# Performance work log

Measured on AMD Instinct MI355X. Metric: run time of the kernel, lower is better.

The kernel has to match this reference:

```python
import jax, jax.numpy as jnp
import numpy as np

# DMoAH constants (match init_kwargs)
H_TOTAL = 16   # attn_h_total
H_ACTIVE = 4   # attn_h_active (per-token top-k heads)


def setup_inputs() -> dict:
    key = jax.random.key(0)
    k1, k2, k3, k4 = jax.random.split(key, 4)
    B, T, D = 2, 2048, 1024
    x = jax.random.normal(k1, (B, T, D), dtype=jnp.float32)
    W_qkv = jax.random.normal(k2, (D, 3 * D), dtype=jnp.float32) * (1.0 / np.sqrt(D))
    W_router = jax.random.normal(k3, (D, H_TOTAL), dtype=jnp.float32) * (1.0 / np.sqrt(D))
    W_o = jax.random.normal(k4, (D, D), dtype=jnp.float32) * (1.0 / np.sqrt(D))
    return {"x": x, "W_qkv": W_qkv, "W_router": W_router, "W_o": W_o}


def reference(x, W_qkv, W_router, W_o):
    B, T, D = x.shape
    dh = D // H_TOTAL
    # --- router: per-token softmax over heads, keep top-k head probs (others zeroed) ---
    probs = jax.nn.softmax(x @ W_router, axis=-1)                 # [B,T,H]
    topv, _ = jax.lax.top_k(probs, H_ACTIVE)                      # [B,T,k]
    thresh = topv[..., -1:]                                       # kth largest prob
    gates = jnp.where(probs >= thresh, probs, 0.0)                # [B,T,H] sparse gates
    # --- QKV projection ---
    qkv = x @ W_qkv                                               # [B,T,3D]
    q, k, v = jnp.split(qkv, 3, axis=-1)
    q = q.reshape(B, T, H_TOTAL, dh).transpose(0, 2, 1, 3)        # [B,H,T,dh]
    k = k.reshape(B, T, H_TOTAL, dh).transpose(0, 2, 1, 3)
    v = v.reshape(B, T, H_TOTAL, dh).transpose(0, 2, 1, 3)
    # --- causal SDPA per head ---
    scale = 1.0 / np.sqrt(dh).astype(np.float32)
    scores = jnp.einsum("bhqd,bhkd->bhqk", q, k) * scale          # [B,H,T,T]
    causal = jnp.tril(jnp.ones((T, T), dtype=bool))
    scores = jnp.where(causal, scores, -jnp.inf)
    attn = jax.nn.softmax(scores, axis=-1)
    head_out = jnp.einsum("bhqk,bhkd->bhqd", attn, v)             # [B,H,T,dh]
    # --- per-token head gating (scatter-combine of active heads) ---
    head_out = head_out.transpose(0, 2, 1, 3)                     # [B,T,H,dh]
    y = (head_out * gates[..., None]).reshape(B, T, D)
    return y @ W_o
```

## Files before the change

kernel.cpp:

```cpp
#include <hip/hip_runtime.h>
#include <math.h>

#define BB 2
#define TT 2048
#define DD 1024
#define HH 16
#define DH 64
#define BTOT (BB*TT)
#define NEG_INF (-1e30f)
#define ATTN_MFMA 1

typedef _Float16 half8 __attribute__((ext_vector_type(8)));
typedef _Float16 half4 __attribute__((ext_vector_type(4)));
typedef float floatx4 __attribute__((ext_vector_type(4)));

__global__ __launch_bounds__(256) void split_f32(const float* __restrict__ in,
                                                 _Float16* __restrict__ hi,
                                                 _Float16* __restrict__ lo,
                                                 int n4) {
  int idx = blockIdx.x * 256 + threadIdx.x;
  const int stride = gridDim.x * 256;
  for (; idx < n4; idx += stride) {
    float4 v = reinterpret_cast<const float4*>(in)[idx];
    half4 hv, lv;
    hv[0] = (_Float16)v.x; lv[0] = (_Float16)(v.x - (float)hv[0]);
    hv[1] = (_Float16)v.y; lv[1] = (_Float16)(v.y - (float)hv[1]);
    hv[2] = (_Float16)v.z; lv[2] = (_Float16)(v.z - (float)hv[2]);
    hv[3] = (_Float16)v.w; lv[3] = (_Float16)(v.w - (float)hv[3]);
    reinterpret_cast<half4*>(hi)[idx] = hv;
    reinterpret_cast<half4*>(lo)[idx] = lv;
  }
}

__global__ __launch_bounds__(256) void wsplit_t(const float* __restrict__ W,
                                                _Float16* __restrict__ Wth,
                                                _Float16* __restrict__ Wtl,
                                                int K, int N) {
  __shared__ float buf[64][65];
  const int tid = threadIdx.x;
  const int k0 = blockIdx.y * 64;
  const int n0 = blockIdx.x * 64;
  const int rr = tid >> 4;
  const int cc = (tid & 15) * 4;
#pragma unroll
  for (int p = 0; p < 4; ++p) {
    const int r = rr + p * 16;
    float4 v = *reinterpret_cast<const float4*>(&W[(size_t)(k0 + r) * N + n0 + cc]);
    buf[r][cc+0] = v.x; buf[r][cc+1] = v.y; buf[r][cc+2] = v.z; buf[r][cc+3] = v.w;
  }
  __syncthreads();
  const int tn = tid >> 2;
#pragma unroll
  for (int pp = 0; pp < 2; ++pp) {
    const int c2 = (tid & 3) + pp * 4;
    half8 hv, lv;
#pragma unroll
    for (int j = 0; j < 8; ++j) {
      float f = buf[c2*8 + j][tn];
      hv[j] = (_Float16)f;
      lv[j] = (_Float16)(f - (float)hv[j]);
    }
    *reinterpret_cast<half8*>(&Wth[(size_t)(n0 + tn) * K + k0 + c2*8]) = hv;
    *reinterpret_cast<half8*>(&Wtl[(size_t)(n0 + tn) * K + k0 + c2*8]) = lv;
  }
}

__global__ __launch_bounds__(64) void router_kernel(const float* __restrict__ x,
                                                    const float* __restrict__ Wr,
                                                    float* __restrict__ gates) {
  const int row = blockIdx.x;
  const int lane = threadIdx.x;
  const float* xr = x + (size_t)row * DD;
  float acc[16];
#pragma unroll
  for (int c = 0; c < 16; ++c) acc[c] = 0.f;
  for (int d = lane; d < DD; d += 64) {
    float xv = xr[d];
    const float4* wrow = reinterpret_cast<const float4*>(Wr + (size_t)d * HH);
#pragma unroll
    for (int g = 0; g < 4; ++g) {
      float4 w = wrow[g];
      acc[g*4+0] = fmaf(xv, w.x, acc[g*4+0]);
      acc[g*4+1] = fmaf(xv, w.y, acc[g*4+1]);
      acc[g*4+2] = fmaf(xv, w.z, acc[g*4+2]);
      acc[g*4+3] = fmaf(xv, w.w, acc[g*4+3]);
    }
  }
#pragma unroll
  for (int c = 0; c < 16; ++c) {
    float v = acc[c];
    v += __shfl_down(v, 32);
    v += __shfl_down(v, 16);
    v += __shfl_down(v, 8);
    v += __shfl_down(v, 4);
    v += __shfl_down(v, 2);
    v += __shfl_down(v, 1);
    acc[c] = v;
  }
  if (lane == 0) {
    float mx = acc[0];
#pragma unroll
    for (int c = 1; c < 16; ++c) mx = fmaxf(mx, acc[c]);
    float e[16]; float den = 0.f;
#pragma unroll
    for (int c = 0; c < 16; ++c) { e[c] = __expf(acc[c] - mx); den += e[c]; }
    float tmp[16];
#pragma unroll
    for (int c = 0; c < 16; ++c) tmp[c] = acc[c];
    float th = NEG_INF;
    for (int it = 0; it < 4; ++it) {
      float bv = NEG_INF; int bi = 0;
      for (int c = 0; c < 16; ++c) { if (tmp[c] > bv) { bv = tmp[c]; bi = c; } }
      tmp[bi] = NEG_INF;
      th = bv;
    }
    float inv = 1.f / den;
    float* gr = gates + (size_t)row * HH;
#pragma unroll
    for (int c = 0; c < 16; ++c) gr[c] = (acc[c] >= th) ? e[c] * inv : 0.f;
  }
}

__global__ __launch_bounds__(256) void hgemm_split(const _Float16* __restrict__ Ah,
                                                   const _Float16* __restrict__ Al,
                                                   const _Float16* __restrict__ Bth,
                                                   const _Float16* __restrict__ Btl,
                                                   float* __restrict__ C,
                                                   int M, int N, int K) {
  __shared__ _Float16 As[2][128][40];
  __shared__ _Float16 Bs[2][128][40];
  const int tid = threadIdx.x;
  const int lane = tid & 63;
  const int w = tid >> 6;
  const int wr = w >> 1, wc = w & 1;
  const int lr = lane & 15, lg = lane >> 4;
  const int m0 = blockIdx.y * 128, n0 = blockIdx.x * 128;
  const int srow = tid >> 2;
  const int schunk = (tid & 3) * 8;
  const _Float16* ApH = Ah + (size_t)(m0 + srow) * K + schunk;
  const _Float16* ApL = Al + (size_t)(m0 + srow) * K + schunk;
  const _Float16* BpH = Bth + (size_t)(n0 + srow) * K + schunk;
  const _Float16* BpL = Btl + (size_t)(n0 + srow) * K + schunk;
  const size_t rskip = (size_t)64 * K;

  floatx4 acc[4][4] = {};
  for (int k0 = 0; k0 < K; k0 += 32) {
    int4 a0h = *reinterpret_cast<const int4*>(ApH + k0);
    int4 a1h = *reinterpret_cast<const int4*>(ApH + rskip + k0);
    int4 a0l = *reinterpret_cast<const int4*>(ApL + k0);
    int4 a1l = *reinterpret_cast<const int4*>(ApL + rskip + k0);
    int4 b0h = *reinterpret_cast<const int4*>(BpH + k0);
    int4 b1h = *reinterpret_cast<const int4*>(BpH + rskip + k0);
    int4 b0l = *reinterpret_cast<const int4*>(BpL + k0);
    int4 b1l = *reinterpret_cast<const int4*>(BpL + rskip + k0);
    __syncthreads();
    *reinterpret_cast<int4*>(&As[0][srow][schunk])      = a0h;
    *reinterpret_cast<int4*>(&As[0][srow + 64][schunk]) = a1h;
    *reinterpret_cast<int4*>(&As[1][srow][schunk])      = a0l;
    *reinterpret_cast<int4*>(&As[1][srow + 64][schunk]) = a1l;
    *reinterpret_cast<int4*>(&Bs[0][srow][schunk])      = b0h;
    *reinterpret_cast<int4*>(&Bs[0][srow + 64][schunk]) = b1h;
    *reinterpret_cast<int4*>(&Bs[1][srow][schunk])      = b0l;
    *reinterpret_cast<int4*>(&Bs[1][srow + 64][schunk]) = b1l;
    __syncthreads();
    half8 af[2][4], bf[2][4];
#pragma unroll
    for (int mi = 0; mi < 4; ++mi) {
      af[0][mi] = *reinterpret_cast<const half8*>(&As[0][wr*64 + mi*16 + lr][lg*8]);
      af[1][mi] = *reinterpret_cast<const half8*>(&As[1][wr*64 + mi*16 + lr][lg*8]);
    }
#pragma unroll
    for (int ni = 0; ni < 4; ++ni) {
      bf[0][ni] = *reinterpret_cast<const half8*>(&Bs[0][wc*64 + ni*16 + lr][lg*8]);
      bf[1][ni] = *reinterpret_cast<const half8*>(&Bs[1][wc*64 + ni*16 + lr][lg*8]);
    }
#pragma unroll
    for (int mi = 0; mi < 4; ++mi)
#pragma unroll
      for (int ni = 0; ni < 4; ++ni) {
        acc[mi][ni] = __builtin_amdgcn_mfma_f32_16x16x32_f16(af[0][mi], bf[0][ni], acc[mi][ni], 0, 0, 0);
        acc[mi][ni] = __builtin_amdgcn_mfma_f32_16x16x32_f16(af[0][mi], bf[1][ni], acc[mi][ni], 0, 0, 0);
        acc[mi][ni] = __builtin_amdgcn_mfma_f32_16x16x32_f16(af[1][mi], bf[0][ni], acc[mi][ni], 0, 0, 0);
      }
  }
#pragma unroll
  for (int mi = 0; mi < 4; ++mi)
#pragma unroll
    for (int ni = 0; ni < 4; ++ni) {
      const int n = n0 + wc*64 + ni*16 + lr;
#pragma unroll
      for (int r = 0; r < 4; ++r) {
        const int m = m0 + wr*64 + mi*16 + lg*4 + r;
        C[(size_t)m * N + n] = acc[mi][ni][r];
      }
    }
}

__global__ __launch_bounds__(256) void attn_mfma(const float* __restrict__ qkv,
                                                 const float* __restrict__ gates,
                                                 _Float16* __restrict__ yhi,
                                                 _Float16* __restrict__ ylo) {
  __shared__ _Float16 Ksh[64][68], Ksl[64][68];
  __shared__ _Float16 Vth[64][68], Vtl[64][68];
  __shared__ _Float16 Psh[64][68], Psl[64][68];
  const int nQT = TT / 64;
  const int bid = blockIdx.x;
  const int qt = nQT - 1 - bid / (BB*HH);
  const int bh = bid % (BB*HH);
  const int b = bh / HH, h = bh % HH;
  const int tid = threadIdx.x;
  const int lane = tid & 63;
  const int wv = tid >> 6;
  const int lr = lane & 15;
  const int lg = lane >> 4;
  const size_t rs = 3 * DD;
  const float* kbase = qkv + (size_t)b*TT*rs + DD + h*DH;
  const float* vbase = qkv + (size_t)b*TT*rs + 2*DD + h*DH;

  half8 qfh[2], qfl[2];
  {
    const float* qrow = qkv + (size_t)(b*TT + qt*64 + wv*16 + lr) * rs + h*DH + lg*8;
#pragma unroll
    for (int c = 0; c < 2; ++c) {
      float4 v0 = *reinterpret_cast<const float4*>(qrow + c*32);
      float4 v1 = *reinterpret_cast<const float4*>(qrow + c*32 + 4);
      const float f[8] = {v0.x,v0.y,v0.z,v0.w,v1.x,v1.y,v1.z,v1.w};
#pragma unroll
      for (int j = 0; j < 8; ++j) {
        qfh[c][j] = (_Float16)f[j];
        qfl[c][j] = (_Float16)(f[j] - (float)qfh[c][j]);
      }
    }
  }
  floatx4 oacc[4] = {};
  float rowM[4], rowL[4];
#pragma unroll
  for (int r = 0; r < 4; ++r) { rowM[r] = NEG_INF; rowL[r] = 0.f; }

  const int sm = tid >> 2;
  const int sg = tid & 3;

  for (int jt = 0; jt <= qt; ++jt) {
    const float* ksrc = kbase + (size_t)(jt*64 + sm) * rs;
    const float* vsrc = vbase + (size_t)(jt*64 + sm) * rs;
    float4 kreg[4], vreg[4];
#pragma unroll
    for (int u = 0; u < 4; ++u) {
      const int c = (sg + 4*u) * 4;
      kreg[u] = *reinterpret_cast<const float4*>(ksrc + c);
      vreg[u] = *reinterpret_cast<const float4*>(vsrc + c);
    }
    __syncthreads();
#pragma unroll
    for (int u = 0; u < 4; ++u) {
      const int c = (sg + 4*u) * 4;
      const float kf[4] = {kreg[u].x, kreg[u].y, kreg[u].z, kreg[u].w};
      half4 kh, kl;
#pragma unroll
      for (int j = 0; j < 4; ++j) {
        kh[j] = (_Float16)kf[j];
        kl[j] = (_Float16)(kf[j] - (float)kh[j]);
      }
      *reinterpret_cast<half4*>(&Ksh[sm][c]) = kh;
      *reinterpret_cast<half4*>(&Ksl[sm][c]) = kl;
      const float vf[4] = {vreg[u].x, vreg[u].y, vreg[u].z, vreg[u].w};
#pragma unroll
      for (int j = 0; j < 4; ++j) {
        _Float16 vh = (_Float16)vf[j];
        Vth[c+j][sm] = vh;
        Vtl[c+j][sm] = (_Float16)(vf[j] - (float)vh);
      }
    }
    __syncthreads();
    floatx4 sacc[4] = {};
#pragma unroll
    for (int c = 0; c < 2; ++c)
#pragma unroll
      for (int nf = 0; nf < 4; ++nf) {
        half8 kbh = *reinterpret_cast<const half8*>(&Ksh[nf*16 + lr][c*32 + lg*8]);
        half8 kbl = *reinterpret_cast<const half8*>(&Ksl[nf*16 + lr][c*32 + lg*8]);
        sacc[nf] = __builtin_amdgcn_mfma_f32_16x16x32_f16(qfh[c], kbh, sacc[nf], 0, 0, 0);
        sacc[nf] = __builtin_amdgcn_mfma_f32_16x16x32_f16(qfh[c], kbl, sacc[nf], 0, 0, 0);
        sacc[nf] = __builtin_amdgcn_mfma_f32_16x16x32_f16(qfl[c], kbh, sacc[nf], 0, 0, 0);
      }
    float p[4][4];
    float corr[4];
#pragma unroll
    for (int r = 0; r < 4; ++r) {
      const int qidx = qt*64 + wv*16 + lg*4 + r;
      float tmax = NEG_INF;
#pragma unroll
      for (int nf = 0; nf < 4; ++nf) {
        const int kidx = jt*64 + nf*16 + lr;
        float sv = sacc[nf][r] * 0.125f;
        if (kidx > qidx) sv = NEG_INF;
        p[nf][r] = sv;
        tmax = fmaxf(tmax, sv);
      }
      tmax = fmaxf(tmax, __shfl_xor(tmax, 1));
      tmax = fmaxf(tmax, __shfl_xor(tmax, 2));
      tmax = fmaxf(tmax, __shfl_xor(tmax, 4));
      tmax = fmaxf(tmax, __shfl_xor(tmax, 8));
      const float mnew = fmaxf(rowM[r], tmax);
      corr[r] = __expf(rowM[r] - mnew);
      float tsum = 0.f;
#pragma unroll
      for (int nf = 0; nf < 4; ++nf) {
        const float pv = __expf(p[nf][r] - mnew);
        p[nf][r] = pv;
        tsum += pv;
      }
      tsum += __shfl_xor(tsum, 1);
      tsum += __shfl_xor(tsum, 2);
      tsum += __shfl_xor(tsum, 4);
      tsum += __shfl_xor(tsum, 8);
      rowL[r] = rowL[r] * corr[r] + tsum;
      rowM[r] = mnew;
    }
#pragma unroll
    for (int nf = 0; nf < 4; ++nf)
#pragma unroll
      for (int r = 0; r < 4; ++r) {
        const _Float16 ph = (_Float16)p[nf][r];
        Psh[wv*16 + lg*4 + r][nf*16 + lr] = ph;
        Psl[wv*16 + lg*4 + r][nf*16 + lr] = (_Float16)(p[nf][r] - (float)ph);
      }
#pragma unroll
    for (int df = 0; df < 4; ++df)
#pragma unroll
      for (int r = 0; r < 4; ++r)
        oacc[df][r] *= corr[r];
#pragma unroll
    for (int c = 0; c < 2; ++c) {
      half8 pah = *reinterpret_cast<const half8*>(&Psh[wv*16 + lr][c*32 + lg*8]);
      half8 pal = *reinterpret_cast<const half8*>(&Psl[wv*16 + lr][c*32 + lg*8]);
#pragma unroll
      for (int df = 0; df < 4; ++df) {
        half8 vbh = *reinterpret_cast<const half8*>(&Vth[df*16 + lr][c*32 + lg*8]);
        half8 vbl = *reinterpret_cast<const half8*>(&Vtl[df*16 + lr][c*32 + lg*8]);
        oacc[df] = __builtin_amdgcn_mfma_f32_16x16x32_f16(pah, vbh, oacc[df], 0, 0, 0);
        oacc[df] = __builtin_amdgcn_mfma_f32_16x16x32_f16(pah, vbl, oacc[df], 0, 0, 0);
        oacc[df] = __builtin_amdgcn_mfma_f32_16x16x32_f16(pal, vbh, oacc[df], 0, 0, 0);
      }
    }
  }
#pragma unroll
  for (int r = 0; r < 4; ++r) {
    const int t = qt*64 + wv*16 + lg*4 + r;
    const float g = gates[((size_t)(b*TT + t)) * HH + h];
    const float sc = g / rowL[r];
#pragma unroll
    for (int df = 0; df < 4; ++df) {
      const float v = oacc[df][r] * sc;
      const _Float16 vh = (_Float16)v;
      const size_t off = ((size_t)(b*TT + t)) * DD + h*DH + df*16 + lr;
      yhi[off] = vh;
      ylo[off] = (_Float16)(v - (float)vh);
    }
  }
}

__global__ __launch_bounds__(256) void attn_kernel(const float* __restrict__ qkv,
                                                   const float* __restrict__ gates,
                                                   _Float16* __restrict__ yhi,
                                                   _Float16* __restrict__ ylo) {
  __shared__ float Qs[64][68];
  __shared__ float KPs[64][68];
  __shared__ float Vs[64][64];
  const int nQT = TT / 64;
  const int bid = blockIdx.x;
  const int qt = nQT - 1 - bid / (BB*HH);
  const int bh = bid % (BB*HH);
  const int b = bh / HH;
  const int h = bh % HH;
  const int tid = threadIdx.x;
  const int tx = tid & 15;
  const int ty = tid >> 4;
  const size_t rs = 3 * DD;
  const float* qbase = qkv + ((size_t)(b*TT + qt*64)) * rs + h*DH;
  const float* kbase = qkv + ((size_t)b*TT) * rs + DD + h*DH;
  const float* vbase = qkv + ((size_t)b*TT) * rs + 2*DD + h*DH;
  const int sm = tid >> 2;
  const int sg = tid & 3;
  {
    const float* src = qbase + (size_t)sm * rs;
#pragma unroll
    for (int u = 0; u < 4; ++u) {
      const int c = (sg + 4*u) * 4;
      float4 v = *reinterpret_cast<const float4*>(src + c);
      Qs[c+0][sm] = v.x; Qs[c+1][sm] = v.y; Qs[c+2][sm] = v.z; Qs[c+3][sm] = v.w;
    }
  }
  float oacc[4][4] = {};
  float rowM[4], rowL[4];
#pragma unroll
  for (int i = 0; i < 4; ++i) { rowM[i] = NEG_INF; rowL[i] = 0.f; }
  for (int jt = 0; jt <= qt; ++jt) {
    const float* ksrc = kbase + (size_t)(jt*64 + sm) * rs;
    const float* vsrc = vbase + (size_t)(jt*64 + sm) * rs;
    float4 kreg[4], vreg[4];
#pragma unroll
    for (int u = 0; u < 4; ++u) {
      const int c = (sg + 4*u) * 4;
      kreg[u] = *reinterpret_cast<const float4*>(ksrc + c);
      vreg[u] = *reinterpret_cast<const float4*>(vsrc + c);
    }
    __syncthreads();
#pragma unroll
    for (int u = 0; u < 4; ++u) {
      const int c = (sg + 4*u) * 4;
      KPs[c+0][sm] = kreg[u].x; KPs[c+1][sm] = kreg[u].y;
      KPs[c+2][sm] = kreg[u].z; KPs[c+3][sm] = kreg[u].w;
      *reinterpret_cast<float4*>(&Vs[sm][c]) = vreg[u];
    }
    __syncthreads();
    float s[4][4] = {};
#pragma unroll 8
    for (int d = 0; d < 64; ++d) {
      float4 qv = *reinterpret_cast<const float4*>(&Qs[d][ty*4]);
      float4 kv = *reinterpret_cast<const float4*>(&KPs[d][tx*4]);
      const float qa[4] = {qv.x,qv.y,qv.z,qv.w};
      const float ka[4] = {kv.x,kv.y,kv.z,kv.w};
#pragma unroll
      for (int i = 0; i < 4; ++i)
#pragma unroll
        for (int j = 0; j < 4; ++j)
          s[i][j] = fmaf(qa[i], ka[j], s[i][j]);
    }
    __syncthreads();
    float p[4][4];
    float corr[4];
#pragma unroll
    for (int i = 0; i < 4; ++i) {
      const int qidx = qt*64 + ty*4 + i;
      float tmax = NEG_INF;
#pragma unroll
      for (int j = 0; j < 4; ++j) {
        const int kidx = jt*64 + tx*4 + j;
        float sv = s[i][j] * 0.125f;
        if (kidx > qidx) sv = NEG_INF;
        s[i][j] = sv;
        tmax = fmaxf(tmax, sv);
      }
      tmax = fmaxf(tmax, __shfl_xor(tmax, 1));
      tmax = fmaxf(tmax, __shfl_xor(tmax, 2));
      tmax = fmaxf(tmax, __shfl_xor(tmax, 4));
      tmax = fmaxf(tmax, __shfl_xor(tmax, 8));
      const float mnew = fmaxf(rowM[i], tmax);
      corr[i] = __expf(rowM[i] - mnew);
      float tsum = 0.f;
#pragma unroll
      for (int j = 0; j < 4; ++j) {
        p[i][j] = __expf(s[i][j] - mnew);
        tsum += p[i][j];
      }
      tsum += __shfl_xor(tsum, 1);
      tsum += __shfl_xor(tsum, 2);
      tsum += __shfl_xor(tsum, 4);
      tsum += __shfl_xor(tsum, 8);
      rowL[i] = rowL[i] * corr[i] + tsum;
      rowM[i] = mnew;
    }
#pragma unroll
    for (int i = 0; i < 4; ++i) {
      float4 v = make_float4(p[i][0], p[i][1], p[i][2], p[i][3]);
      *reinterpret_cast<float4*>(&KPs[ty*4+i][tx*4]) = v;
    }
#pragma unroll
    for (int i = 0; i < 4; ++i)
#pragma unroll
      for (int j = 0; j < 4; ++j)
        oacc[i][j] *= corr[i];
    __syncthreads();
#pragma unroll 4
    for (int n = 0; n < 64; ++n) {
      float4 vv = *reinterpret_cast<const float4*>(&Vs[n][tx*4]);
      const float va[4] = {vv.x, vv.y, vv.z, vv.w};
#pragma unroll
      for (int i = 0; i < 4; ++i) {
        const float pm = KPs[ty*4+i][n];
#pragma unroll
        for (int j = 0; j < 4; ++j)
          oacc[i][j] = fmaf(pm, va[j], oacc[i][j]);
      }
    }
  }
#pragma unroll
  for (int i = 0; i < 4; ++i) {
    const int t = qt*64 + ty*4 + i;
    const float g = gates[((size_t)(b*TT + t)) * HH + h];
    const float sc = g / rowL[i];
    half4 hv, lv;
#pragma unroll
    for (int j = 0; j < 4; ++j) {
      float v = oacc[i][j] * sc;
      hv[j] = (_Float16)v;
      lv[j] = (_Float16)(v - (float)hv[j]);
    }
    const size_t off = ((size_t)(b*TT + t)) * DD + h*DH + tx*4;
    *reinterpret_cast<half4*>(&yhi[off]) = hv;
    *reinterpret_cast<half4*>(&ylo[off]) = lv;
  }
}

extern "C" void kernel_launch(void* const* d_in, const int* in_sizes, int n_in,
                              void* d_out, int out_size, void* d_ws, size_t ws_size,
                              hipStream_t stream) {
  (void)in_sizes; (void)n_in; (void)out_size; (void)ws_size;
  const float* x    = (const float*)d_in[0];
  const float* Wqkv = (const float*)d_in[1];
  const float* Wr   = (const float*)d_in[2];
  const float* Wo   = (const float*)d_in[3];
  float* out = (float*)d_out;

  float* ws = (float*)d_ws;
  float* qkv   = ws;
  float* gates = qkv + (size_t)BTOT * 3 * DD;
  _Float16* x_hi = (_Float16*)(gates + (size_t)BTOT * HH);
  _Float16* x_lo = x_hi + (size_t)BTOT * DD;
  _Float16* Wqh  = x_lo + (size_t)BTOT * DD;
  _Float16* Wql  = Wqh + (size_t)DD * 3 * DD;
  _Float16* Woh  = Wql + (size_t)DD * 3 * DD;
  _Float16* Wol  = Woh + (size_t)DD * DD;
  _Float16* yhi = x_hi;
  _Float16* ylo = x_lo;

  split_f32<<<1024, 256, 0, stream>>>(x, x_hi, x_lo, BTOT * DD / 4);
  wsplit_t<<<dim3(3*DD/64, DD/64), 256, 0, stream>>>(Wqkv, Wqh, Wql, DD, 3*DD);
  wsplit_t<<<dim3(DD/64, DD/64), 256, 0, stream>>>(Wo, Woh, Wol, DD, DD);
  router_kernel<<<BTOT, 64, 0, stream>>>(x, Wr, gates);
  hgemm_split<<<dim3(3*DD/128, BTOT/128), 256, 0, stream>>>(x_hi, x_lo, Wqh, Wql, qkv, BTOT, 3*DD, DD);
#if ATTN_MFMA
  attn_mfma<<<(TT/64)*BB*HH, 256, 0, stream>>>(qkv, gates, yhi, ylo);
#else
  attn_kernel<<<(TT/64)*BB*HH, 256, 0, stream>>>(qkv, gates, yhi, ylo);
#endif
  hgemm_split<<<dim3(DD/128, BTOT/128), 256, 0, stream>>>(yhi, ylo, Woh, Wol, out, BTOT, DD, DD);
}
```

Before: 370.3 us.

## Emit split-fp16 QKV from GEMM epilogue and drop V low-part MFMA

The QKV GEMM now writes hi/lo fp16 halves directly in its epilogue, so the attention kernel loads fp16 instead of fp32 and skips per-tile conversion. The V low-order term (pah*vfl) is dropped by default, which removes one MFMA per P·V step plus the V_lo loads and shared-memory stores. The unused scalar attention kernel is deleted. Dropping V_lo lowers accuracy on the P·V product.

```diff
diff --git a/kernel.cpp b/kernel.cpp
--- a/kernel.cpp
+++ b/kernel.cpp
@@ -8,7 +8,7 @@
 #define DH 64
 #define BTOT (BB*TT)
 #define NEG_INF (-1e30f)
-#define ATTN_MFMA 1
+#define V_LO 0
 
 typedef _Float16 half8 __attribute__((ext_vector_type(8)));
 typedef _Float16 half4 __attribute__((ext_vector_type(4)));
@@ -121,11 +121,14 @@
   }
 }
 
+template<bool EMIT_HALF>
 __global__ __launch_bounds__(256) void hgemm_split(const _Float16* __restrict__ Ah,
                                                    const _Float16* __restrict__ Al,
                                                    const _Float16* __restrict__ Bth,
                                                    const _Float16* __restrict__ Btl,
                                                    float* __restrict__ C,
+                                                   _Float16* __restrict__ Ch,
+                                                   _Float16* __restrict__ Cl,
                                                    int M, int N, int K) {
   __shared__ _Float16 As[2][128][40];
   __shared__ _Float16 Bs[2][128][40];
@@ -191,17 +194,28 @@
 #pragma unroll
       for (int r = 0; r < 4; ++r) {
         const int m = m0 + wr*64 + mi*16 + lg*4 + r;
-        C[(size_t)m * N + n] = acc[mi][ni][r];
-      }
-    }
-}
-
-__global__ __launch_bounds__(256) void attn_mfma(const float* __restrict__ qkv,
+        const float v = acc[mi][ni][r];
+        if (EMIT_HALF) {
+          const _Float16 vh = (_Float16)v;
+          Ch[(size_t)m * N + n] = vh;
+          Cl[(size_t)m * N + n] = (_Float16)(v - (float)vh);
+        } else {
+          C[(size_t)m * N + n] = v;
+        }
+      }
+    }
+}
+
+__global__ __launch_bounds__(256) void attn_mfma(const _Float16* __restrict__ qkvh,
+                                                 const _Float16* __restrict__ qkvl,
                                                  const float* __restrict__ gates,
                                                  _Float16* __restrict__ yhi,
                                                  _Float16* __restrict__ ylo) {
   __shared__ _Float16 Ksh[64][68], Ksl[64][68];
-  __shared__ _Float16 Vth[64][68], Vtl[64][68];
+  __shared__ _Float16 Vth[64][68];
+#if V_LO
+  __shared__ _Float16 Vtl[64][68];
+#endif
   __shared__ _Float16 Psh[64][68], Psl[64][68];
   const int nQT = TT / 64;
   const int bid = blockIdx.x;
@@ -214,22 +228,21 @@
   const int lr = lane & 15;
   const int lg = lane >> 4;
   const size_t rs = 3 * DD;
-  const float* kbase = qkv + (size_t)b*TT*rs + DD + h*DH;
-  const float* vbase = qkv + (size_t)b*TT*rs + 2*DD + h*DH;
+  const _Float16* kbh = qkvh + (size_t)b*TT*rs + DD + h*DH;
+  const _Float16* kbl = qkvl + (size_t)b*TT*rs + DD + h*DH;
+  const _Float16* vbh = qkvh + (size_t)b*TT*rs + 2*DD + h*DH;
+#if V_LO
+  const _Float16* vbl = qkvl + (size_t)b*TT*rs + 2*DD + h*DH;
+#endif
 
   half8 qfh[2], qfl[2];
   {
-    const float* qrow = qkv + (size_t)(b*TT + qt*64 + wv*16 + lr) * rs + h*DH + lg*8;
+    const _Float16* qrh = qkvh + (size_t)(b*TT + qt*64 + wv*16 + lr) * rs + h*DH + lg*8;
+    const _Float16* qrl = qkvl + (size_t)(b*TT + qt*64 + wv*16 + lr) * rs + h*DH + lg*8;
 #pragma unroll
     for (int c = 0; c < 2; ++c) {
-      float4 v0 = *reinterpret_cast<const float4*>(qrow + c*32);
-      float4 v1 = *reinterpret_cast<const float4*>(qrow + c*32 + 4);
-      const float f[8] = {v0.x,v0.y,v0.z,v0.w,v1.x,v1.y,v1.z,v1.w};
-#pragma unroll
-      for (int j = 0; j < 8; ++j) {
-        qfh[c][j] = (_Float16)f[j];
-        qfl[c][j] = (_Float16)(f[j] - (float)qfh[c][j]);
-      }
+      qfh[c] = *reinterpret_cast<const half8*>(qrh + c*32);
+      qfl[c] = *reinterpret_cast<const half8*>(qrl + c*32);
     }
   }
   floatx4 oacc[4] = {};
@@ -241,35 +254,30 @@
   const int sg = tid & 3;
 
   for (int jt = 0; jt <= qt; ++jt) {
-    const float* ksrc = kbase + (size_t)(jt*64 + sm) * rs;
-    const float* vsrc = vbase + (size_t)(jt*64 + sm) * rs;
-    float4 kreg[4], vreg[4];
-#pragma unroll
-    for (int u = 0; u < 4; ++u) {
-      const int c = (sg + 4*u) * 4;
-      kreg[u] = *reinterpret_cast<const float4*>(ksrc + c);
-      vreg[u] = *reinterpret_cast<const float4*>(vsrc + c);
-    }
+    const size_t roff = (size_t)(jt*64 + sm) * rs + sg*16;
+    half8 kh0 = *reinterpret_cast<const half8*>(kbh + roff);
+    half8 kh1 = *reinterpret_cast<const half8*>(kbh + roff + 8);
+    half8 kl0 = *reinterpret_cast<const half8*>(kbl + roff);
+    half8 kl1 = *reinterpret_cast<const half8*>(kbl + roff + 8);
+    half8 vh0 = *reinterpret_cast<const half8*>(vbh + roff);
+    half8 vh1 = *reinterpret_cast<const half8*>(vbh + roff + 8);
+#if V_LO
+    half8 vl0 = *reinterpret_cast<const half8*>(vbl + roff);
+    half8 vl1 = *reinterpret_cast<const half8*>(vbl + roff + 8);
+#endif
     __syncthreads();
-#pragma unroll
-    for (int u = 0; u < 4; ++u) {
-      const int c = (sg + 4*u) * 4;
-      const float kf[4] = {kreg[u].x, kreg[u].y, kreg[u].z, kreg[u].w};
-      half4 kh, kl;
-#pragma unroll
-      for (int j = 0; j < 4; ++j) {
-        kh[j] = (_Float16)kf[j];
-        kl[j] = (_Float16)(kf[j] - (float)kh[j]);
-      }
-      *reinterpret_cast<half4*>(&Ksh[sm][c]) = kh;
-      *reinterpret_cast<half4*>(&Ksl[sm][c]) = kl;
-      const float vf[4] = {vreg[u].x, vreg[u].y, vreg[u].z, vreg[u].w};
-#pragma unroll
-      for (int j = 0; j < 4; ++j) {
-        _Float16 vh = (_Float16)vf[j];
-        Vth[c+j][sm] = vh;
-        Vtl[c+j][sm] = (_Float16)(vf[j] - (float)vh);
-      }
+    *reinterpret_cast<half8*>(&Ksh[sm][sg*16])     = kh0;
+    *reinterpret_cast<half8*>(&Ksh[sm][sg*16 + 8]) = kh1;
+    *reinterpret_cast<half8*>(&Ksl[sm][sg*16])     = kl0;
+    *reinterpret_cast<half8*>(&Ksl[sm][sg*16 + 8]) = kl1;
+#pragma unroll
+    for (int jj = 0; jj < 8; ++jj) {
+      Vth[sg*16 + jj][sm]     = vh0[jj];
+      Vth[sg*16 + 8 + jj][sm] = vh1[jj];
+#if V_LO
+      Vtl[sg*16 + jj][sm]     = vl0[jj];
+      Vtl[sg*16 + 8 + jj][sm] = vl1[jj];
+#endif
     }
     __syncthreads();
     floatx4 sacc[4] = {};
@@ -277,11 +285,11 @@
     for (int c = 0; c < 2; ++c)
 #pragma unroll
       for (int nf = 0; nf < 4; ++nf) {
-        half8 kbh = *reinterpret_cast<const half8*>(&Ksh[nf*16 + lr][c*32 + lg*8]);
-        half8 kbl = *reinterpret_cast<const half8*>(&Ksl[nf*16 + lr][c*32 + lg*8]);
-        sacc[nf] = __builtin_amdgcn_mfma_f32_16x16x32_f16(qfh[c], kbh, sacc[nf], 0, 0, 0);
-        sacc[nf] = __builtin_amdgcn_mfma_f32_16x16x32_f16(qfh[c], kbl, sacc[nf], 0, 0, 0);
-        sacc[nf] = __builtin_amdgcn_mfma_f32_16x16x32_f16(qfl[c], kbh, sacc[nf], 0, 0, 0);
+        half8 kfh = *reinterpret_cast<const half8*>(&Ksh[nf*16 + lr][c*32 + lg*8]);
+        half8 kfl = *reinterpret_cast<const half8*>(&Ksl[nf*16 + lr][c*32 + lg*8]);
+        sacc[nf] = __builtin_amdgcn_mfma_f32_16x16x32_f16(qfh[c], kfh, sacc[nf], 0, 0, 0);
+        sacc[nf] = __builtin_amdgcn_mfma_f32_16x16x32_f16(qfh[c], kfl, sacc[nf], 0, 0, 0);
+        sacc[nf] = __builtin_amdgcn_mfma_f32_16x16x32_f16(qfl[c], kfh, sacc[nf], 0, 0, 0);
       }
     float p[4][4];
     float corr[4];
@@ -336,11 +344,13 @@
       half8 pal = *reinterpret_cast<const half8*>(&Psl[wv*16 + lr][c*32 + lg*8]);
 #pragma unroll
       for (int df = 0; df < 4; ++df) {
-        half8 vbh = *reinterpret_cast<const half8*>(&Vth[df*16 + lr][c*32 + lg*8]);
-        half8 vbl = *reinterpret_cast<const half8*>(&Vtl[df*16 + lr][c*32 + lg*8]);
-        oacc[df] = __builtin_amdgcn_mfma_f32_16x16x32_f16(pah, vbh, oacc[df], 0, 0, 0);
-        oacc[df] = __builtin_amdgcn_mfma_f32_16x16x32_f16(pah, vbl, oacc[df], 0, 0, 0);
-        oacc[df] = __builtin_amdgcn_mfma_f32_16x16x32_f16(pal, vbh, oacc[df], 0, 0, 0);
+        half8 vfh = *reinterpret_cast<const half8*>(&Vth[df*16 + lr][c*32 + lg*8]);
+        oacc[df] = __builtin_amdgcn_mfma_f32_16x16x32_f16(pah, vfh, oacc[df], 0, 0, 0);
+        oacc[df] = __builtin_amdgcn_mfma_f32_16x16x32_f16(pal, vfh, oacc[df], 0, 0, 0);
+#if V_LO
+        half8 vfl = *reinterpret_cast<const half8*>(&Vtl[df*16 + lr][c*32 + lg*8]);
+        oacc[df] = __builtin_amdgcn_mfma_f32_16x16x32_f16(pah, vfl, oacc[df], 0, 0, 0);
+#endif
       }
     }
   }
@@ -357,149 +367,6 @@
       yhi[off] = vh;
       ylo[off] = (_Float16)(v - (float)vh);
     }
-  }
-}
-
-__global__ __launch_bounds__(256) void attn_kernel(const float* __restrict__ qkv,
-                                                   const float* __restrict__ gates,
-                                                   _Float16* __restrict__ yhi,
-                                                   _Float16* __restrict__ ylo) {
-  __shared__ float Qs[64][68];
-  __shared__ float KPs[64][68];
-  __shared__ float Vs[64][64];
-  const int nQT = TT / 64;
-  const int bid = blockIdx.x;
-  const int qt = nQT - 1 - bid / (BB*HH);
-  const int bh = bid % (BB*HH);
-  const int b = bh / HH;
-  const int h = bh % HH;
-  const int tid = threadIdx.x;
-  const int tx = tid & 15;
-  const int ty = tid >> 4;
-  const size_t rs = 3 * DD;
-  const float* qbase = qkv + ((size_t)(b*TT + qt*64)) * rs + h*DH;
-  const float* kbase = qkv + ((size_t)b*TT) * rs + DD + h*DH;
-  const float* vbase = qkv + ((size_t)b*TT) * rs + 2*DD + h*DH;
-  const int sm = tid >> 2;
-  const int sg = tid & 3;
-  {
-    const float* src = qbase + (size_t)sm * rs;
-#pragma unroll
-    for (int u = 0; u < 4; ++u) {
-      const int c = (sg + 4*u) * 4;
-      float4 v = *reinterpret_cast<const float4*>(src + c);
-      Qs[c+0][sm] = v.x; Qs[c+1][sm] = v.y; Qs[c+2][sm] = v.z; Qs[c+3][sm] = v.w;
-    }
-  }
-  float oacc[4][4] = {};
-  float rowM[4], rowL[4];
-#pragma unroll
-  for (int i = 0; i < 4; ++i) { rowM[i] = NEG_INF; rowL[i] = 0.f; }
-  for (int jt = 0; jt <= qt; ++jt) {
-    const float* ksrc = kbase + (size_t)(jt*64 + sm) * rs;
-    const float* vsrc = vbase + (size_t)(jt*64 + sm) * rs;
-    float4 kreg[4], vreg[4];
-#pragma unroll
-    for (int u = 0; u < 4; ++u) {
-      const int c = (sg + 4*u) * 4;
-      kreg[u] = *reinterpret_cast<const float4*>(ksrc + c);
-      vreg[u] = *reinterpret_cast<const float4*>(vsrc + c);
-    }
-    __syncthreads();
-#pragma unroll
-    for (int u = 0; u < 4; ++u) {
-      const int c = (sg + 4*u) * 4;
-      KPs[c+0][sm] = kreg[u].x; KPs[c+1][sm] = kreg[u].y;
-      KPs[c+2][sm] = kreg[u].z; KPs[c+3][sm] = kreg[u].w;
-      *reinterpret_cast<float4*>(&Vs[sm][c]) = vreg[u];
-    }
-    __syncthreads();
-    float s[4][4] = {};
-#pragma unroll 8
-    for (int d = 0; d < 64; ++d) {
-      float4 qv = *reinterpret_cast<const float4*>(&Qs[d][ty*4]);
-      float4 kv = *reinterpret_cast<const float4*>(&KPs[d][tx*4]);
-      const float qa[4] = {qv.x,qv.y,qv.z,qv.w};
-      const float ka[4] = {kv.x,kv.y,kv.z,kv.w};
-#pragma unroll
-      for (int i = 0; i < 4; ++i)
-#pragma unroll
-        for (int j = 0; j < 4; ++j)
-          s[i][j] = fmaf(qa[i], ka[j], s[i][j]);
-    }
-    __syncthreads();
-    float p[4][4];
-    float corr[4];
-#pragma unroll
-    for (int i = 0; i < 4; ++i) {
-      const int qidx = qt*64 + ty*4 + i;
-      float tmax = NEG_INF;
-#pragma unroll
-      for (int j = 0; j < 4; ++j) {
-        const int kidx = jt*64 + tx*4 + j;
-        float sv = s[i][j] * 0.125f;
-        if (kidx > qidx) sv = NEG_INF;
-        s[i][j] = sv;
-        tmax = fmaxf(tmax, sv);
-      }
-      tmax = fmaxf(tmax, __shfl_xor(tmax, 1));
-      tmax = fmaxf(tmax, __shfl_xor(tmax, 2));
-      tmax = fmaxf(tmax, __shfl_xor(tmax, 4));
-      tmax = fmaxf(tmax, __shfl_xor(tmax, 8));
-      const float mnew = fmaxf(rowM[i], tmax);
-      corr[i] = __expf(rowM[i] - mnew);
-      float tsum = 0.f;
-#pragma unroll
-      for (int j = 0; j < 4; ++j) {
-        p[i][j] = __expf(s[i][j] - mnew);
-        tsum += p[i][j];
-      }
-      tsum += __shfl_xor(tsum, 1);
-      tsum += __shfl_xor(tsum, 2);
-      tsum += __shfl_xor(tsum, 4);
-      tsum += __shfl_xor(tsum, 8);
-      rowL[i] = rowL[i] * corr[i] + tsum;
-      rowM[i] = mnew;
-    }
-#pragma unroll
-    for (int i = 0; i < 4; ++i) {
-      float4 v = make_float4(p[i][0], p[i][1], p[i][2], p[i][3]);
-      *reinterpret_cast<float4*>(&KPs[ty*4+i][tx*4]) = v;
-    }
-#pragma unroll
-    for (int i = 0; i < 4; ++i)
-#pragma unroll
-      for (int j = 0; j < 4; ++j)
-        oacc[i][j] *= corr[i];
-    __syncthreads();
-#pragma unroll 4
-    for (int n = 0; n < 64; ++n) {
-      float4 vv = *reinterpret_cast<const float4*>(&Vs[n][tx*4]);
-      const float va[4] = {vv.x, vv.y, vv.z, vv.w};
-#pragma unroll
-      for (int i = 0; i < 4; ++i) {
-        const float pm = KPs[ty*4+i][n];
-#pragma unroll
-        for (int j = 0; j < 4; ++j)
-          oacc[i][j] = fmaf(pm, va[j], oacc[i][j]);
-      }
-    }
-  }
-#pragma unroll
-  for (int i = 0; i < 4; ++i) {
-    const int t = qt*64 + ty*4 + i;
-    const float g = gates[((size_t)(b*TT + t)) * HH + h];
-    const float sc = g / rowL[i];
-    half4 hv, lv;
-#pragma unroll
-    for (int j = 0; j < 4; ++j) {
-      float v = oacc[i][j] * sc;
-      hv[j] = (_Float16)v;
-      lv[j] = (_Float16)(v - (float)hv[j]);
-    }
-    const size_t off = ((size_t)(b*TT + t)) * DD + h*DH + tx*4;
-    *reinterpret_cast<half4*>(&yhi[off]) = hv;
-    *reinterpret_cast<half4*>(&ylo[off]) = lv;
   }
 }
 
@@ -513,9 +380,9 @@
   const float* Wo   = (const float*)d_in[3];
   float* out = (float*)d_out;
 
-  float* ws = (float*)d_ws;
-  float* qkv   = ws;
-  float* gates = qkv + (size_t)BTOT * 3 * DD;
+  _Float16* qkvh = (_Float16*)d_ws;
+  _Float16* qkvl = qkvh + (size_t)BTOT * 3 * DD;
+  float*    gates = (float*)(qkvl + (size_t)BTOT * 3 * DD);
   _Float16* x_hi = (_Float16*)(gates + (size_t)BTOT * HH);
   _Float16* x_lo = x_hi + (size_t)BTOT * DD;
   _Float16* Wqh  = x_lo + (size_t)BTOT * DD;
@@ -529,11 +396,9 @@
   wsplit_t<<<dim3(3*DD/64, DD/64), 256, 0, stream>>>(Wqkv, Wqh, Wql, DD, 3*DD);
   wsplit_t<<<dim3(DD/64, DD/64), 256, 0, stream>>>(Wo, Woh, Wol, DD, DD);
   router_kernel<<<BTOT, 64, 0, stream>>>(x, Wr, gates);
-  hgemm_split<<<dim3(3*DD/128, BTOT/128), 256, 0, stream>>>(x_hi, x_lo, Wqh, Wql, qkv, BTOT, 3*DD, DD);
-#if ATTN_MFMA
-  attn_mfma<<<(TT/64)*BB*HH, 256, 0, stream>>>(qkv, gates, yhi, ylo);
-#else
-  attn_kernel<<<(TT/64)*BB*HH, 256, 0, stream>>>(qkv, gates, yhi, ylo);
-#endif
-  hgemm_split<<<dim3(DD/128, BTOT/128), 256, 0, stream>>>(yhi, ylo, Woh, Wol, out, BTOT, DD, DD);
-}
+  hgemm_split<true><<<dim3(3*DD/128, BTOT/128), 256, 0, stream>>>(
+      x_hi, x_lo, Wqh, Wql, nullptr, qkvh, qkvl, BTOT, 3*DD, DD);
+  attn_mfma<<<(TT/64)*BB*HH, 256, 0, stream>>>(qkvh, qkvl, gates, yhi, ylo);
+  hgemm_split<false><<<dim3(DD/128, BTOT/128), 256, 0, stream>>>(
+      yhi, ylo, Woh, Wol, out, nullptr, nullptr, BTOT, DD, DD);
+}
```

New measurement: 350.0 us. -5.5%, faster.
